# Kernel tuning notes

Measured on AMD Instinct MI355X. Metric: run time of the kernel, lower is better.

Reference implementation:

```python
import jax, jax.numpy as jnp
import numpy as np

NUM_EMBEDDINGS = 1024
EMBEDDING_DIM = 64
COMMITMENT_COST = 0.25


def setup_inputs() -> dict:
    key = jax.random.key(0)
    k1, k2 = jax.random.split(key)
    z = jax.random.normal(k1, (32, 64, 64, 64), dtype=jnp.float32)  # [B, C=D, H, W]
    # module initializes embedding ~ Uniform(-1/K, 1/K)
    embedding = jax.random.uniform(
        k2, (NUM_EMBEDDINGS, EMBEDDING_DIM), dtype=jnp.float32,
        minval=-1.0 / NUM_EMBEDDINGS, maxval=1.0 / NUM_EMBEDDINGS)
    return {"z": z, "embedding": embedding}


def reference(z, embedding):
    B, C, H, W = z.shape
    K = embedding.shape[0]
    zp = jnp.transpose(z, (0, 2, 3, 1))          # b h w c
    z_flat = zp.reshape(-1, C)                   # [N, D]

    # L2 distances: ||z||^2 + ||e||^2 - 2 z e^T   -> [N, K]
    distances = (jnp.sum(z_flat * z_flat, axis=1, keepdims=True)
                 + jnp.sum(embedding * embedding, axis=1)
                 - 2.0 * jnp.matmul(z_flat, embedding.T))
    encoding_indices = jnp.argmin(distances, axis=1)          # [N] int

    # one-hot matmul lookup == direct gather (same math)
    quantized = embedding[encoding_indices].reshape(zp.shape)  # b h w c

    e_latent_loss = jnp.mean((jax.lax.stop_gradient(quantized) - zp) ** 2)
    q_latent_loss = jnp.mean((quantized - jax.lax.stop_gradient(zp)) ** 2)
    loss = q_latent_loss + COMMITMENT_COST * e_latent_loss

    # straight-through estimator
    quantized_st = zp + jax.lax.stop_gradient(quantized - zp)
    quantized_out = jnp.transpose(quantized_st, (0, 3, 1, 2))  # b c h w

    # perplexity from average code usage
    N = z_flat.shape[0]
    counts = jnp.zeros((K,), dtype=jnp.float32).at[encoding_indices].add(1.0)
    avg_probs = counts / N
    perplexity = jnp.exp(-jnp.sum(avg_probs * jnp.log(avg_probs + 1e-10)))

    return quantized_out, loss, perplexity, encoding_indices
```

## Files before the change

kernel.cpp:

```cpp
#include <hip/hip_runtime.h>
#include <math.h>


#define NROWS 131072
#define KCODES 1024
#define DDIM 64
#define CAP 16

typedef __attribute__((ext_vector_type(8))) short short8v;
typedef __attribute__((ext_vector_type(4))) float f32x4;

__device__ __forceinline__ float nofuse(float x) {
    asm("" : "+v"(x));
    return x;
}

template <typename F>
__device__ __forceinline__ float pairwise64_sq(F load) {
    float r[8];
#pragma unroll
    for (int j = 0; j < 8; j++) {
        float v = load(j);
        r[j] = nofuse(v * v);
    }
#pragma unroll
    for (int i = 8; i < 64; i += 8) {
#pragma unroll
        for (int j = 0; j < 8; j++) {
            float v = load(i + j);
            r[j] = r[j] + nofuse(v * v);
        }
    }
    return ((r[0] + r[1]) + (r[2] + r[3])) + ((r[4] + r[5]) + (r[6] + r[7]));
}

__device__ __forceinline__ unsigned short bf16_rne(float x) {
    unsigned u = __float_as_uint(x);
    u += 0x7FFFu + ((u >> 16) & 1u);
    return (unsigned short)(u >> 16);
}

__global__ __launch_bounds__(256) void kE(const float* __restrict__ emb,
                                          float* __restrict__ ee,
                                          unsigned short* __restrict__ eh_p) {
    int k = blockIdx.x * 256 + threadIdx.x;
    if (k >= KCODES) return;
    const float* er = emb + (size_t)k * DDIM;
    ee[k] = pairwise64_sq([&](int i) { return er[i]; });
#pragma unroll
    for (int i = 0; i < DDIM; i++) eh_p[(size_t)k * DDIM + i] = bf16_rne(er[i]);
}

#define MFMA_BF16(acc, a, b) \
    acc = __builtin_amdgcn_mfma_f32_16x16x32_bf16(a, b, acc, 0, 0, 0)

#define DOT_TILE(ti, B0, B1, ACT)                                       \
    {                                                                   \
        const int codeL = code0 + (ti) * 16 + (l & 15);                 \
        const float eev = ee_s[codeL];                                  \
        _Pragma("unroll") for (int rt = 0; rt < 4; rt++) {              \
            f32x4 acc = {0.f, 0.f, 0.f, 0.f};                           \
            MFMA_BF16(acc, ah[rt][0], B0);                              \
            MFMA_BF16(acc, ah[rt][1], B1);                              \
            _Pragma("unroll") for (int r = 0; r < 4; r++) {             \
                float sv = fmaf(-2.0f, acc[r], eev);                    \
                ACT(rt, r, sv, codeL);                                  \
            }                                                           \
        }                                                               \
    }

#define ACT_MIN(rt, r, sv, code) rm[rt][r] = fminf(rm[rt][r], sv);
#define ACT_COLLECT(rt, r, sv, code)                                    \
    if (sv <= thr_r[rt][r]) {                                           \
        int row_ = rt * 16 + ((l >> 4) << 2) + r;                       \
        int pos_ = atomicAdd(&cnt_s[row_], 1);                          \
        if (pos_ < CAP) cand_s[row_][pos_] = (unsigned short)(code);    \
    }

#define PRE_B(ti)                                                       \
    {                                                                   \
        const unsigned short* p_ =                                      \
            ebase + (size_t)((ti) * 16 + (l & 15)) * 64 + kg;           \
        pb0[(ti) % 3] = *(const short8v*)p_;                            \
        pb1[(ti) % 3] = *(const short8v*)(p_ + 32);                     \
    }

__global__ __launch_bounds__(256, 4) void kA2(
    const float* __restrict__ z, const float* __restrict__ emb,
    const float* __restrict__ ee, const unsigned short* __restrict__ eh_p,
    int* __restrict__ counts, float* __restrict__ out_idx,
    float* __restrict__ out_q, double* __restrict__ loss_sum) {
    __shared__ float zt[64][65];
    __shared__ float ee_s[KCODES];
    __shared__ float zz_s[64];
    __shared__ float wq_s[64];
    __shared__ float rmw_s[4][64];
    __shared__ float thr_s[64];
    __shared__ int cnt_s[64];
    __shared__ unsigned short cand_s[64][CAP];
    __shared__ int idx_s[64];
    __shared__ double wred[4];

    const int tid = threadIdx.x;
    const int blk = blockIdx.x;
    const int n0 = blk * 64;
    const int b = blk >> 6;
    const int h = blk & 63;

    const float* zb = z + (size_t)b * 262144 + (size_t)h * 64;
#pragma unroll
    for (int it = 0; it < 4; it++) {
        int idx = it * 256 + tid;
        int d = idx >> 4, w4 = (idx & 15) * 4;
        float4 v = *(const float4*)(zb + (size_t)d * 4096 + w4);
        zt[w4 + 0][d] = v.x;
        zt[w4 + 1][d] = v.y;
        zt[w4 + 2][d] = v.z;
        zt[w4 + 3][d] = v.w;
    }
    for (int i = tid; i < KCODES; i += 256) ee_s[i] = ee[i];
    __syncthreads();

    if (tid < 64) {
        const int w = tid;
        zz_s[w] = pairwise64_sq([&](int i) { return zt[w][i]; });
        float s = 0.0f;
#pragma unroll
        for (int i = 0; i < 64; i++) s += fabsf(zt[w][i]);
        wq_s[w] = fmaf(2e-5f, s, 1e-4f);
        cnt_s[w] = 0;
    }
    __syncthreads();

    const int wv = tid >> 6;
    const int l = tid & 63;
    const int kg = (l >> 4) * 8;
    const int code0 = wv * 256;

    short8v ah[4][2];
#pragma unroll
    for (int rt = 0; rt < 4; rt++) {
        const int arow = rt * 16 + (l & 15);
#pragma unroll
        for (int kt = 0; kt < 2; kt++) {
#pragma unroll
            for (int i = 0; i < 8; i++)
                ah[rt][kt][i] = (short)bf16_rne(zt[arow][kt * 32 + kg + i]);
        }
    }

    const unsigned short* ebase = eh_p + (size_t)code0 * 64;

    float rm[4][4];
#pragma unroll
    for (int rt = 0; rt < 4; rt++)
#pragma unroll
        for (int r = 0; r < 4; r++) rm[rt][r] = INFINITY;
    {
        short8v pb0[3], pb1[3];
        PRE_B(0)
        PRE_B(1)
#pragma unroll
        for (int ti = 0; ti < 16; ti++) {
            if (ti + 2 < 16) PRE_B(ti + 2)
            DOT_TILE(ti, pb0[ti % 3], pb1[ti % 3], ACT_MIN)
        }
    }
#pragma unroll
    for (int rt = 0; rt < 4; rt++)
#pragma unroll
        for (int r = 0; r < 4; r++) {
            float v = rm[rt][r];
            v = fminf(v, __shfl_xor(v, 1, 64));
            v = fminf(v, __shfl_xor(v, 2, 64));
            v = fminf(v, __shfl_xor(v, 4, 64));
            v = fminf(v, __shfl_xor(v, 8, 64));
            rm[rt][r] = v;
        }
    if ((l & 15) == 0) {
#pragma unroll
        for (int rt = 0; rt < 4; rt++)
#pragma unroll
            for (int r = 0; r < 4; r++)
                rmw_s[wv][rt * 16 + ((l >> 4) << 2) + r] = rm[rt][r];
    }
    __syncthreads();
    if (tid < 64) {
        float m01 = fminf(rmw_s[0][tid], rmw_s[1][tid]);
        float m23 = fminf(rmw_s[2][tid], rmw_s[3][tid]);
        thr_s[tid] = fminf(m01, m23) + wq_s[tid];
    }
    __syncthreads();

    float thr_r[4][4];
#pragma unroll
    for (int rt = 0; rt < 4; rt++)
#pragma unroll
        for (int r = 0; r < 4; r++)
            thr_r[rt][r] = thr_s[rt * 16 + ((l >> 4) << 2) + r];

    {
        short8v pb0[3], pb1[3];
        PRE_B(0)
        PRE_B(1)
#pragma unroll
        for (int ti = 0; ti < 16; ti++) {
            if (ti + 2 < 16) PRE_B(ti + 2)
            DOT_TILE(ti, pb0[ti % 3], pb1[ti % 3], ACT_COLLECT)
        }
    }
    __syncthreads();

    if (tid < 64) {
        const int w = tid;
        const float zzv = zz_s[w];
        float bv = INFINITY;
        int bi = 0;
        const int nc = cnt_s[w];
        if (nc > CAP) {
            for (int k = 0; k < KCODES; k++) {
                const float4* er = (const float4*)(emb + (size_t)k * 64);
                float dot = 0.0f;
#pragma unroll
                for (int q = 0; q < 16; q++) {
                    float4 e4 = er[q];
                    dot = __builtin_fmaf(zt[w][4 * q + 0], e4.x, dot);
                    dot = __builtin_fmaf(zt[w][4 * q + 1], e4.y, dot);
                    dot = __builtin_fmaf(zt[w][4 * q + 2], e4.z, dot);
                    dot = __builtin_fmaf(zt[w][4 * q + 3], e4.w, dot);
                }
                float tt = zzv + ee_s[k];
                float dv = tt - 2.0f * dot;
                if (dv < bv || (dv == bv && k < bi)) { bv = dv; bi = k; }
            }
        } else {
            for (int j = 0; j < nc; j++) {
                const int k = cand_s[w][j];
                const float4* er = (const float4*)(emb + (size_t)k * 64);
                float dot = 0.0f;
#pragma unroll
                for (int q = 0; q < 16; q++) {
                    float4 e4 = er[q];
                    dot = __builtin_fmaf(zt[w][4 * q + 0], e4.x, dot);
                    dot = __builtin_fmaf(zt[w][4 * q + 1], e4.y, dot);
                    dot = __builtin_fmaf(zt[w][4 * q + 2], e4.z, dot);
                    dot = __builtin_fmaf(zt[w][4 * q + 3], e4.w, dot);
                }
                float tt = zzv + ee_s[k];
                float dv = tt - 2.0f * dot;
                if (dv < bv || (dv == bv && k < bi)) { bv = dv; bi = k; }
            }
        }
        idx_s[w] = bi;
        out_idx[n0 + w] = (float)bi;
        atomicAdd(&counts[bi], 1);
    }
    __syncthreads();

    float* qb = out_q + (size_t)b * 262144 + (size_t)h * 64;
    double dsum = 0.0;
    for (int i = tid; i < 4096; i += 256) {
        int c = i >> 6, w = i & 63;
        float q = emb[(size_t)idx_s[w] * 64 + c];
        float zv = zt[w][c];
        qb[(size_t)c * 4096 + w] = q;
        float df = q - zv;
        float s = df * df;
        dsum += (double)s;
    }
    for (int off = 32; off > 0; off >>= 1) dsum += __shfl_down(dsum, off, 64);
    if ((tid & 63) == 0) wred[tid >> 6] = dsum;
    __syncthreads();
    if (tid == 0) {
        double tot = (wred[0] + wred[1]) + (wred[2] + wred[3]);
        atomicAdd(loss_sum, tot);
    }
}

__global__ __launch_bounds__(1024) void kC(const int* __restrict__ counts,
                                           const double* __restrict__ loss_sum,
                                           float* __restrict__ out_loss,
                                           float* __restrict__ out_perp) {
    __shared__ float wr[16];
    const int tid = threadIdx.x;
    float p = (float)counts[tid] * (1.0f / 131072.0f);
    float v = p + 1e-10f;
    float term = p * logf(v);
    float s = term;
    for (int off = 32; off > 0; off >>= 1) s += __shfl_down(s, off, 64);
    if ((tid & 63) == 0) wr[tid >> 6] = s;
    __syncthreads();
    if (tid == 0) {
        float tot = 0.0f;
#pragma unroll
        for (int j = 0; j < 16; j++) tot += wr[j];
        out_perp[0] = expf(-tot);
        double L = *loss_sum / 8388608.0;
        float Lf = (float)L;
        out_loss[0] = Lf + 0.25f * Lf;
    }
}

extern "C" void kernel_launch(void* const* d_in, const int* in_sizes, int n_in,
                              void* d_out, int out_size, void* d_ws, size_t ws_size,
                              hipStream_t stream) {
    const float* z = (const float*)d_in[0];
    const float* emb = (const float*)d_in[1];
    float* out = (float*)d_out;
    float* out_q = out;
    float* out_loss = out + 8388608;
    float* out_perp = out + 8388609;
    float* out_idx = out + 8388610;

    char* ws = (char*)d_ws;
    double* loss_sum = (double*)ws;
    int* counts = (int*)(ws + 64);
    float* ee = (float*)(ws + 64 + 4096);
    unsigned short* eh_p = (unsigned short*)(ws + 64 + 8192);

    hipMemsetAsync(d_ws, 0, 64 + 4096, stream);
    kE<<<4, 256, 0, stream>>>(emb, ee, eh_p);
    kA2<<<2048, 256, 0, stream>>>(z, emb, ee, eh_p, counts, out_idx, out_q,
                                  loss_sum);
    kC<<<1, 1024, 0, stream>>>(counts, loss_sum, out_loss, out_perp);
}
```

Before: 133.8 us.

## Use single-wave blocks that scan all codes per wave

Shrinks the main kernel from four waves per block, each scanning a quarter of the codebook, to one wave per block that scans all 1024 codes for its 64 rows. This removes the cross-wave min reduction through shared memory, the ee staging into LDS, and several block barriers. Overflow rows now get a wave-cooperative exhaustive search, and the quantized write-out is done per lane with float4 codebook reads. The trade-off is four times more serial MFMA work per wave with the same 2048 blocks, so fewer waves are resident to hide latency.

```diff
diff --git a/kernel.cpp b/kernel.cpp
--- a/kernel.cpp
+++ b/kernel.cpp
@@ -56,8 +56,8 @@
 
 #define DOT_TILE(ti, B0, B1, ACT)                                       \
     {                                                                   \
-        const int codeL = code0 + (ti) * 16 + (l & 15);                 \
-        const float eev = ee_s[codeL];                                  \
+        const int codeL = (ti) * 16 + (l & 15);                         \
+        const float eev = ee[codeL];                                    \
         _Pragma("unroll") for (int rt = 0; rt < 4; rt++) {              \
             f32x4 acc = {0.f, 0.f, 0.f, 0.f};                           \
             MFMA_BF16(acc, ah[rt][0], B0);                              \
@@ -80,37 +80,34 @@
 #define PRE_B(ti)                                                       \
     {                                                                   \
         const unsigned short* p_ =                                      \
-            ebase + (size_t)((ti) * 16 + (l & 15)) * 64 + kg;           \
-        pb0[(ti) % 3] = *(const short8v*)p_;                            \
-        pb1[(ti) % 3] = *(const short8v*)(p_ + 32);                     \
-    }
-
-__global__ __launch_bounds__(256, 4) void kA2(
+            eh_p + (size_t)((ti) * 16 + (l & 15)) * 64 + kg;            \
+        pb0[(ti) & 3] = *(const short8v*)p_;                            \
+        pb1[(ti) & 3] = *(const short8v*)(p_ + 32);                     \
+    }
+
+__global__ __launch_bounds__(64) void kA2(
     const float* __restrict__ z, const float* __restrict__ emb,
     const float* __restrict__ ee, const unsigned short* __restrict__ eh_p,
     int* __restrict__ counts, float* __restrict__ out_idx,
     float* __restrict__ out_q, double* __restrict__ loss_sum) {
     __shared__ float zt[64][65];
-    __shared__ float ee_s[KCODES];
     __shared__ float zz_s[64];
     __shared__ float wq_s[64];
-    __shared__ float rmw_s[4][64];
     __shared__ float thr_s[64];
     __shared__ int cnt_s[64];
     __shared__ unsigned short cand_s[64][CAP];
-    __shared__ int idx_s[64];
-    __shared__ double wred[4];
-
-    const int tid = threadIdx.x;
+
+    const int l = threadIdx.x;
     const int blk = blockIdx.x;
     const int n0 = blk * 64;
     const int b = blk >> 6;
     const int h = blk & 63;
+    const int kg = (l >> 4) * 8;
 
     const float* zb = z + (size_t)b * 262144 + (size_t)h * 64;
 #pragma unroll
-    for (int it = 0; it < 4; it++) {
-        int idx = it * 256 + tid;
+    for (int it = 0; it < 16; it++) {
+        int idx = it * 64 + l;
         int d = idx >> 4, w4 = (idx & 15) * 4;
         float4 v = *(const float4*)(zb + (size_t)d * 4096 + w4);
         zt[w4 + 0][d] = v.x;
@@ -118,24 +115,24 @@
         zt[w4 + 2][d] = v.z;
         zt[w4 + 3][d] = v.w;
     }
-    for (int i = tid; i < KCODES; i += 256) ee_s[i] = ee[i];
-    __syncthreads();
-
-    if (tid < 64) {
-        const int w = tid;
-        zz_s[w] = pairwise64_sq([&](int i) { return zt[w][i]; });
-        float s = 0.0f;
-#pragma unroll
-        for (int i = 0; i < 64; i++) s += fabsf(zt[w][i]);
-        wq_s[w] = fmaf(2e-5f, s, 1e-4f);
-        cnt_s[w] = 0;
-    }
-    __syncthreads();
-
-    const int wv = tid >> 6;
-    const int l = tid & 63;
-    const int kg = (l >> 4) * 8;
-    const int code0 = wv * 256;
+    __syncthreads();
+
+    const float zz = pairwise64_sq([&](int i) { return zt[l][i]; });
+    zz_s[l] = zz;
+    {
+        float sa[8];
+#pragma unroll
+        for (int j = 0; j < 8; j++) sa[j] = fabsf(zt[l][j]);
+#pragma unroll
+        for (int i = 8; i < 64; i += 8)
+#pragma unroll
+            for (int j = 0; j < 8; j++) sa[j] += fabsf(zt[l][i + j]);
+        float s = ((sa[0] + sa[1]) + (sa[2] + sa[3])) +
+                  ((sa[4] + sa[5]) + (sa[6] + sa[7]));
+        wq_s[l] = fmaf(2e-5f, s, 1e-4f);
+    }
+    cnt_s[l] = 0;
+    __syncthreads();
 
     short8v ah[4][2];
 #pragma unroll
@@ -149,21 +146,19 @@
         }
     }
 
-    const unsigned short* ebase = eh_p + (size_t)code0 * 64;
-
     float rm[4][4];
 #pragma unroll
     for (int rt = 0; rt < 4; rt++)
 #pragma unroll
         for (int r = 0; r < 4; r++) rm[rt][r] = INFINITY;
     {
-        short8v pb0[3], pb1[3];
+        short8v pb0[4], pb1[4];
         PRE_B(0)
         PRE_B(1)
-#pragma unroll
-        for (int ti = 0; ti < 16; ti++) {
-            if (ti + 2 < 16) PRE_B(ti + 2)
-            DOT_TILE(ti, pb0[ti % 3], pb1[ti % 3], ACT_MIN)
+#pragma unroll 4
+        for (int ti = 0; ti < 64; ti++) {
+            if (ti < 62) PRE_B(ti + 2)
+            DOT_TILE(ti, pb0[ti & 3], pb1[ti & 3], ACT_MIN)
         }
     }
 #pragma unroll
@@ -181,14 +176,10 @@
 #pragma unroll
         for (int rt = 0; rt < 4; rt++)
 #pragma unroll
-            for (int r = 0; r < 4; r++)
-                rmw_s[wv][rt * 16 + ((l >> 4) << 2) + r] = rm[rt][r];
-    }
-    __syncthreads();
-    if (tid < 64) {
-        float m01 = fminf(rmw_s[0][tid], rmw_s[1][tid]);
-        float m23 = fminf(rmw_s[2][tid], rmw_s[3][tid]);
-        thr_s[tid] = fminf(m01, m23) + wq_s[tid];
+            for (int r = 0; r < 4; r++) {
+                int row = rt * 16 + ((l >> 4) << 2) + r;
+                thr_s[row] = rm[rt][r] + wq_s[row];
+            }
     }
     __syncthreads();
 
@@ -200,81 +191,94 @@
             thr_r[rt][r] = thr_s[rt * 16 + ((l >> 4) << 2) + r];
 
     {
-        short8v pb0[3], pb1[3];
+        short8v pb0[4], pb1[4];
         PRE_B(0)
         PRE_B(1)
-#pragma unroll
-        for (int ti = 0; ti < 16; ti++) {
-            if (ti + 2 < 16) PRE_B(ti + 2)
-            DOT_TILE(ti, pb0[ti % 3], pb1[ti % 3], ACT_COLLECT)
-        }
-    }
-    __syncthreads();
-
-    if (tid < 64) {
-        const int w = tid;
-        const float zzv = zz_s[w];
-        float bv = INFINITY;
-        int bi = 0;
-        const int nc = cnt_s[w];
-        if (nc > CAP) {
-            for (int k = 0; k < KCODES; k++) {
-                const float4* er = (const float4*)(emb + (size_t)k * 64);
-                float dot = 0.0f;
-#pragma unroll
-                for (int q = 0; q < 16; q++) {
-                    float4 e4 = er[q];
-                    dot = __builtin_fmaf(zt[w][4 * q + 0], e4.x, dot);
-                    dot = __builtin_fmaf(zt[w][4 * q + 1], e4.y, dot);
-                    dot = __builtin_fmaf(zt[w][4 * q + 2], e4.z, dot);
-                    dot = __builtin_fmaf(zt[w][4 * q + 3], e4.w, dot);
-                }
-                float tt = zzv + ee_s[k];
-                float dv = tt - 2.0f * dot;
-                if (dv < bv || (dv == bv && k < bi)) { bv = dv; bi = k; }
+#pragma unroll 4
+        for (int ti = 0; ti < 64; ti++) {
+            if (ti < 62) PRE_B(ti + 2)
+            DOT_TILE(ti, pb0[ti & 3], pb1[ti & 3], ACT_COLLECT)
+        }
+    }
+    __syncthreads();
+
+    const int nc = cnt_s[l];
+    float bv = INFINITY;
+    int bi = 0;
+    if (nc <= CAP) {
+        for (int j = 0; j < nc; j++) {
+            const int k = cand_s[l][j];
+            const float4* er = (const float4*)(emb + (size_t)k * 64);
+            float dot = 0.0f;
+#pragma unroll
+            for (int q = 0; q < 16; q++) {
+                float4 e4 = er[q];
+                dot = __builtin_fmaf(zt[l][4 * q + 0], e4.x, dot);
+                dot = __builtin_fmaf(zt[l][4 * q + 1], e4.y, dot);
+                dot = __builtin_fmaf(zt[l][4 * q + 2], e4.z, dot);
+                dot = __builtin_fmaf(zt[l][4 * q + 3], e4.w, dot);
             }
-        } else {
-            for (int j = 0; j < nc; j++) {
-                const int k = cand_s[w][j];
-                const float4* er = (const float4*)(emb + (size_t)k * 64);
-                float dot = 0.0f;
-#pragma unroll
-                for (int q = 0; q < 16; q++) {
-                    float4 e4 = er[q];
-                    dot = __builtin_fmaf(zt[w][4 * q + 0], e4.x, dot);
-                    dot = __builtin_fmaf(zt[w][4 * q + 1], e4.y, dot);
-                    dot = __builtin_fmaf(zt[w][4 * q + 2], e4.z, dot);
-                    dot = __builtin_fmaf(zt[w][4 * q + 3], e4.w, dot);
-                }
-                float tt = zzv + ee_s[k];
-                float dv = tt - 2.0f * dot;
-                if (dv < bv || (dv == bv && k < bi)) { bv = dv; bi = k; }
+            float tt = zz + ee[k];
+            float dv = tt - 2.0f * dot;
+            if (dv < bv || (dv == bv && k < bi)) { bv = dv; bi = k; }
+        }
+    }
+    unsigned long long ovf = __ballot(nc > CAP);
+    while (ovf) {
+        int row = __ffsll(ovf) - 1;
+        ovf &= (ovf - 1);
+        const float zzr = zz_s[row];
+        float lbv = INFINITY;
+        int lbi = 0;
+        for (int c = 0; c < 16; c++) {
+            const int k = c * 64 + l;
+            const float4* er = (const float4*)(emb + (size_t)k * 64);
+            float dot = 0.0f;
+#pragma unroll
+            for (int q = 0; q < 16; q++) {
+                float4 e4 = er[q];
+                dot = __builtin_fmaf(zt[row][4 * q + 0], e4.x, dot);
+                dot = __builtin_fmaf(zt[row][4 * q + 1], e4.y, dot);
+                dot = __builtin_fmaf(zt[row][4 * q + 2], e4.z, dot);
+                dot = __builtin_fmaf(zt[row][4 * q + 3], e4.w, dot);
             }
-        }
-        idx_s[w] = bi;
-        out_idx[n0 + w] = (float)bi;
-        atomicAdd(&counts[bi], 1);
-    }
-    __syncthreads();
-
+            float tt = zzr + ee[k];
+            float dv = tt - 2.0f * dot;
+            if (dv < lbv || (dv == lbv && k < lbi)) { lbv = dv; lbi = k; }
+        }
+#pragma unroll
+        for (int off = 1; off < 64; off <<= 1) {
+            float ov = __shfl_xor(lbv, off, 64);
+            int oi = __shfl_xor(lbi, off, 64);
+            if (ov < lbv || (ov == lbv && oi < lbi)) { lbv = ov; lbi = oi; }
+        }
+        if (l == row) { bv = lbv; bi = lbi; }
+    }
+
+    out_idx[n0 + l] = (float)bi;
+    atomicAdd(&counts[bi], 1);
+
+    const float4* eq = (const float4*)(emb + (size_t)bi * 64);
     float* qb = out_q + (size_t)b * 262144 + (size_t)h * 64;
     double dsum = 0.0;
-    for (int i = tid; i < 4096; i += 256) {
-        int c = i >> 6, w = i & 63;
-        float q = emb[(size_t)idx_s[w] * 64 + c];
-        float zv = zt[w][c];
-        qb[(size_t)c * 4096 + w] = q;
-        float df = q - zv;
-        float s = df * df;
-        dsum += (double)s;
+#pragma unroll 4
+    for (int j = 0; j < 16; j++) {
+        float4 q4 = eq[j];
+        qb[(size_t)(4 * j + 0) * 4096 + l] = q4.x;
+        qb[(size_t)(4 * j + 1) * 4096 + l] = q4.y;
+        qb[(size_t)(4 * j + 2) * 4096 + l] = q4.z;
+        qb[(size_t)(4 * j + 3) * 4096 + l] = q4.w;
+        float d0 = q4.x - zt[l][4 * j + 0];
+        float d1 = q4.y - zt[l][4 * j + 1];
+        float d2 = q4.z - zt[l][4 * j + 2];
+        float d3 = q4.w - zt[l][4 * j + 3];
+        dsum += (double)(d0 * d0);
+        dsum += (double)(d1 * d1);
+        dsum += (double)(d2 * d2);
+        dsum += (double)(d3 * d3);
     }
     for (int off = 32; off > 0; off >>= 1) dsum += __shfl_down(dsum, off, 64);
-    if ((tid & 63) == 0) wred[tid >> 6] = dsum;
-    __syncthreads();
-    if (tid == 0) {
-        double tot = (wred[0] + wred[1]) + (wred[2] + wred[3]);
-        atomicAdd(loss_sum, tot);
-    }
+    if (l == 0) atomicAdd(loss_sum, dsum);
 }
 
 __global__ __launch_bounds__(1024) void kC(const int* __restrict__ counts,
@@ -320,7 +324,7 @@
 
     hipMemsetAsync(d_ws, 0, 64 + 4096, stream);
     kE<<<4, 256, 0, stream>>>(emb, ee, eh_p);
-    kA2<<<2048, 256, 0, stream>>>(z, emb, ee, eh_p, counts, out_idx, out_q,
-                                  loss_sum);
+    kA2<<<2048, 64, 0, stream>>>(z, emb, ee, eh_p, counts, out_idx, out_q,
+                                 loss_sum);
     kC<<<1, 1024, 0, stream>>>(counts, loss_sum, out_loss, out_perp);
 }
```

After: 167.9 us. 1.25x slower.
